# Kernel tuning notes

Hardware: AMD Instinct MI355X
Metric: run time of the kernel (lower is better)

## Reference

```python
import jax, jax.numpy as jnp
import numpy as np

NEG_SLOPE = 0.2


def _attn_layer(x, src, dst, W, a, n_nodes):
    # x: (N, Cin), W: (Cout, Cin) torch Linear convention, a: (2*Cout,)
    h = x @ W.T                                  # (N, Cout)
    H = h.shape[-1]
    # cat([x_i, x_j]) @ a  ==  h[dst] @ a[:H] + h[src] @ a[H:]
    s_i = h @ a[:H]                              # (N,)
    s_j = h @ a[H:]                              # (N,)
    score = s_i[dst] + s_j[src]                  # (E,)
    alpha = jax.nn.leaky_relu(score, NEG_SLOPE)
    # segment softmax over destination nodes
    amax = jax.ops.segment_max(alpha, dst, num_segments=n_nodes)
    amax = jnp.where(jnp.isfinite(amax), amax, 0.0)
    ex = jnp.exp(alpha - amax[dst])
    denom = jax.ops.segment_sum(ex, dst, num_segments=n_nodes)
    alpha = ex / denom[dst]                      # (E,)
    msg = h[src] * alpha[:, None]                # (E, Cout)
    sums = jax.ops.segment_sum(msg, dst, num_segments=n_nodes)
    cnt = jax.ops.segment_sum(jnp.ones_like(alpha), dst, num_segments=n_nodes)
    return sums / jnp.maximum(cnt, 1.0)[:, None]  # mean aggregation


def setup_inputs() -> dict:
    key = jax.random.key(0)
    ks = jax.random.split(key, 8)
    B, N, C, H, E = 16, 2048, 256, 256, 262144
    NT = B * N
    temporal_features = jax.random.normal(ks[0], (B, N, C), dtype=jnp.float32)
    edge_index = jax.random.randint(ks[1], (2, E), 0, NT, dtype=jnp.int64)
    sc = 1.0 / np.sqrt(C)
    W1 = jax.random.normal(ks[2], (H, C), dtype=jnp.float32) * sc
    a1 = jax.random.normal(ks[3], (2 * H,), dtype=jnp.float32) * sc
    W2 = jax.random.normal(ks[4], (H, H), dtype=jnp.float32) * sc
    a2 = jax.random.normal(ks[5], (2 * H,), dtype=jnp.float32) * sc
    W3 = jax.random.normal(ks[6], (H, H), dtype=jnp.float32) * sc
    a3 = jax.random.normal(ks[7], (2 * H,), dtype=jnp.float32) * sc
    return {"temporal_features": temporal_features, "edge_index": edge_index,
            "W1": W1, "a1": a1, "W2": W2, "a2": a2, "W3": W3, "a3": a3}


def reference(temporal_features, edge_index, W1, a1, W2, a2, W3, a3):
    B, N, C = temporal_features.shape
    n_nodes = B * N
    src, dst = edge_index[0], edge_index[1]  # x_j = x[src], x_i = x[dst]
    x = temporal_features.reshape(n_nodes, C)
    for W, a in ((W1, a1), (W2, a2), (W3, a3)):
        x = _attn_layer(x, src, dst, W, a, n_nodes)
        x = jax.nn.elu(x)
    return x.reshape(B, N, -1)
```

## Files before the change

kernel.cpp:

```cpp
#include <hip/hip_runtime.h>
#include <math.h>
#include <stdint.h>


typedef float f32x4 __attribute__((ext_vector_type(4)));
typedef _Float16 f16x8 __attribute__((ext_vector_type(8)));
typedef _Float16 f16x4 __attribute__((ext_vector_type(4)));


__global__ __launch_bounds__(256) void convert_f16(const float* __restrict__ src,
                                                   _Float16* __restrict__ dstp)
{
    const int i = (blockIdx.x * 256 + threadIdx.x) * 8;
    float4 a = *(const float4*)&src[i];
    float4 b = *(const float4*)&src[i + 4];
    f16x8 o = {(_Float16)a.x, (_Float16)a.y, (_Float16)a.z, (_Float16)a.w,
               (_Float16)b.x, (_Float16)b.y, (_Float16)b.z, (_Float16)b.w};
    *(f16x8*)&dstp[i] = o;
}


#define SWZ(row, byte) ((byte) ^ (((row) & 7) << 4))

__global__ __launch_bounds__(512) void gemm_f16(const _Float16* __restrict__ X,
                                                const _Float16* __restrict__ Wh,
                                                const float* __restrict__ avec,
                                                _Float16* __restrict__ Hout,
                                                float* __restrict__ si,
                                                float* __restrict__ sj)
{
    __shared__ __align__(16) unsigned char smem[49152];
    char* Xs = (char*)smem;
    char* Wl = (char*)smem + 16384;
    float (*Es)[260] = (float (*)[260])smem;

    const int tid  = threadIdx.x;
    const int lane = tid & 63;
    const int w    = tid >> 6;
    const int wr   = w >> 2;
    const int wc   = w & 3;
    const int ln   = lane & 15;
    const int kq   = lane >> 4;
    const int m0   = blockIdx.x * 128;

    const int xr = tid >> 2;
    const int xc = tid & 3;
    const int wrow = tid >> 1;
    const int wcb  = (tid & 1) * 64;

    const _Float16* Xg = X  + (size_t)(m0 + xr) * 256 + xc * 16;
    const _Float16* Wg = Wh + (size_t)wrow * 256 + wcb / 2;
    char* XsW = Xs + SWZ(xr, xr * 128 + xc * 32);
    char* XsW2 = Xs + SWZ(xr, xr * 128 + xc * 32 + 16);
    char* WlW0 = Wl + SWZ(wrow, wrow * 128 + wcb + 0);
    char* WlW1 = Wl + SWZ(wrow, wrow * 128 + wcb + 16);
    char* WlW2 = Wl + SWZ(wrow, wrow * 128 + wcb + 32);
    char* WlW3 = Wl + SWZ(wrow, wrow * 128 + wcb + 48);

    f32x4 acc[4][4] = {};

    for (int k0 = 0; k0 < 256; k0 += 64) {
        f16x8 x0 = *(const f16x8*)&Xg[k0];
        f16x8 x1 = *(const f16x8*)&Xg[k0 + 8];
        f16x8 w0 = *(const f16x8*)&Wg[k0];
        f16x8 w1 = *(const f16x8*)&Wg[k0 + 8];
        f16x8 w2 = *(const f16x8*)&Wg[k0 + 16];
        f16x8 w3 = *(const f16x8*)&Wg[k0 + 24];
        *(f16x8*)XsW  = x0;  *(f16x8*)XsW2 = x1;
        *(f16x8*)WlW0 = w0;  *(f16x8*)WlW1 = w1;
        *(f16x8*)WlW2 = w2;  *(f16x8*)WlW3 = w3;
        __syncthreads();

#pragma unroll
        for (int kk = 0; kk < 2; ++kk) {
            f16x8 af[4], bf[4];
#pragma unroll
            for (int i = 0; i < 4; ++i) {
                const int row = wr * 64 + i * 16 + ln;
                af[i] = *(const f16x8*)(Xs + SWZ(row, row * 128 + kk * 64 + kq * 16));
            }
#pragma unroll
            for (int j = 0; j < 4; ++j) {
                const int row = wc * 64 + j * 16 + ln;
                bf[j] = *(const f16x8*)(Wl + SWZ(row, row * 128 + kk * 64 + kq * 16));
            }
#pragma unroll
            for (int i = 0; i < 4; ++i)
#pragma unroll
                for (int j = 0; j < 4; ++j)
                    acc[i][j] = __builtin_amdgcn_mfma_f32_16x16x32_f16(af[i], bf[j], acc[i][j], 0, 0, 0);
        }
        __syncthreads();
    }

    const int er = tid >> 5;
    const int ec = tid & 31;
    for (int g = 0; g < 8; ++g) {
        if (wr == (g >> 2)) {
            const int i = g & 3;
#pragma unroll
            for (int j = 0; j < 4; ++j) {
                const int col = wc * 64 + j * 16 + ln;
#pragma unroll
                for (int q = 0; q < 4; ++q)
                    Es[kq * 4 + q][col] = acc[i][j][q];
            }
        }
        __syncthreads();
        const int grow = m0 + g * 16 + er;
        const int c0 = ec * 8;
        f32x4 v0 = *(const f32x4*)&Es[er][c0];
        f32x4 v1 = *(const f32x4*)&Es[er][c0 + 4];
        f16x8 ho = {(_Float16)v0[0], (_Float16)v0[1], (_Float16)v0[2], (_Float16)v0[3],
                    (_Float16)v1[0], (_Float16)v1[1], (_Float16)v1[2], (_Float16)v1[3]};
        *(f16x8*)&Hout[(size_t)grow * 256 + c0] = ho;

        f32x4 al0 = *(const f32x4*)&avec[c0];
        f32x4 al1 = *(const f32x4*)&avec[c0 + 4];
        f32x4 ah0 = *(const f32x4*)&avec[256 + c0];
        f32x4 ah1 = *(const f32x4*)&avec[256 + c0 + 4];
        float d0 = v0[0]*al0[0] + v0[1]*al0[1] + v0[2]*al0[2] + v0[3]*al0[3]
                 + v1[0]*al1[0] + v1[1]*al1[1] + v1[2]*al1[2] + v1[3]*al1[3];
        float d1 = v0[0]*ah0[0] + v0[1]*ah0[1] + v0[2]*ah0[2] + v0[3]*ah0[3]
                 + v1[0]*ah1[0] + v1[1]*ah1[1] + v1[2]*ah1[2] + v1[3]*ah1[3];
#pragma unroll
        for (int d = 16; d; d >>= 1) {
            d0 += __shfl_xor(d0, d);
            d1 += __shfl_xor(d1, d);
        }
        if (ec == 0) { si[grow] = d0; sj[grow] = d1; }
        __syncthreads();
    }
}


__global__ void zero_int(int* p, int n)
{
    int i = blockIdx.x * blockDim.x + threadIdx.x;
    if (i < n) p[i] = 0;
}

__global__ void hist_kernel(const int* __restrict__ dst, int* __restrict__ cnt, int E)
{
    int e = blockIdx.x * blockDim.x + threadIdx.x;
    if (e < E) atomicAdd(&cnt[dst[e]], 1);
}

__global__ __launch_bounds__(1024) void scan_part(const int* __restrict__ cnt,
                                                  int* __restrict__ off,
                                                  int* __restrict__ bsum)
{
    __shared__ int buf[1024];
    const int tid = threadIdx.x;
    const int g = blockIdx.x * 1024 + tid;
    int v = cnt[g];
    buf[tid] = v;
    __syncthreads();
#pragma unroll
    for (int d = 1; d < 1024; d <<= 1) {
        int t = (tid >= d) ? buf[tid - d] : 0;
        __syncthreads();
        buf[tid] += t;
        __syncthreads();
    }
    off[g] = buf[tid] - v;
    if (tid == 1023) bsum[blockIdx.x] = buf[1023];
}

__global__ void scan_bsum(int* bsum, int nb)
{
    __shared__ int b[64];
    const int tid = threadIdx.x;
    b[tid] = (tid < nb) ? bsum[tid] : 0;
    __syncthreads();
    if (tid == 0) {
        int a = 0;
        for (int i = 0; i < nb; ++i) { int t = b[i]; b[i] = a; a += t; }
    }
    __syncthreads();
    if (tid < nb) bsum[tid] = b[tid];
}

__global__ __launch_bounds__(1024) void scan_add(const int* __restrict__ bsum,
                                                 int* __restrict__ off,
                                                 int* __restrict__ cursor,
                                                 int NT, int E)
{
    const int tid = threadIdx.x;
    const int g = blockIdx.x * 1024 + tid;
    int v = off[g] + bsum[blockIdx.x];
    off[g] = v;
    cursor[g] = v;
    if (g == 0) off[NT] = E;
}

__global__ void scatter_kernel(const int* __restrict__ src,
                               const int* __restrict__ dst,
                               int* __restrict__ cursor,
                               int* __restrict__ ssrc, int E)
{
    int e = blockIdx.x * blockDim.x + threadIdx.x;
    if (e < E) {
        int p = atomicAdd(&cursor[dst[e]], 1);
        ssrc[p] = src[e];
    }
}


__device__ __forceinline__ float bcast_f(float x, int l)
{
    return __uint_as_float(__builtin_amdgcn_readlane(__float_as_uint(x), l));
}

template <int F16OUT>
__global__ __launch_bounds__(256) void aggregate(const _Float16* __restrict__ Hh,
                                                 const float* __restrict__ si,
                                                 const float* __restrict__ sj,
                                                 const int* __restrict__ off,
                                                 const int* __restrict__ ssrc,
                                                 void* __restrict__ outv,
                                                 int n_nodes)
{
    const int v = (blockIdx.x * 256 + threadIdx.x) >> 6;
    const int lane = threadIdx.x & 63;
    if (v >= n_nodes) return;

    const int e0 = off[v], e1 = off[v + 1];
    const int deg = e1 - e0;
    f32x4 acc = {0.f, 0.f, 0.f, 0.f};

    if (deg > 0 && deg <= 64) {
        const float siv = si[v];
        const int idx = e0 + lane;
        const bool on = idx < e1;
        int s = 0;
        float scv = -1e30f;
        if (on) {
            s = ssrc[idx];
            float t = siv + sj[s];
            scv = (t >= 0.f) ? t : 0.2f * t;
        }
        float m = scv;
#pragma unroll
        for (int d = 32; d; d >>= 1) m = fmaxf(m, __shfl_xor(m, d));
        float wv = on ? __expf(scv - m) : 0.f;
        float den = wv;
#pragma unroll
        for (int d = 32; d; d >>= 1) den += __shfl_xor(den, d);

        const int c4 = lane * 4;
        for (int eo = 0; eo < deg; eo += 4) {
            const int l1 = (eo + 1 < 63) ? eo + 1 : 63;
            const int l2 = (eo + 2 < 63) ? eo + 2 : 63;
            const int l3 = (eo + 3 < 63) ? eo + 3 : 63;
            const int s0 = __builtin_amdgcn_readlane(s, eo);
            const int s1 = __builtin_amdgcn_readlane(s, l1);
            const int s2 = __builtin_amdgcn_readlane(s, l2);
            const int s3 = __builtin_amdgcn_readlane(s, l3);
            const float w0 = bcast_f(wv, eo);
            const float w1 = bcast_f(wv, l1);
            const float w2 = bcast_f(wv, l2);
            const float w3 = bcast_f(wv, l3);
            const f16x4 v0 = *(const f16x4*)&Hh[(size_t)s0 * 256 + c4];
            const f16x4 v1 = *(const f16x4*)&Hh[(size_t)s1 * 256 + c4];
            const f16x4 v2 = *(const f16x4*)&Hh[(size_t)s2 * 256 + c4];
            const f16x4 v3 = *(const f16x4*)&Hh[(size_t)s3 * 256 + c4];
#pragma unroll
            for (int q = 0; q < 4; ++q)
                acc[q] += w0 * (float)v0[q] + w1 * (float)v1[q]
                        + w2 * (float)v2[q] + w3 * (float)v3[q];
        }
        const float inv = 1.f / (den * (float)deg);
#pragma unroll
        for (int q = 0; q < 4; ++q) acc[q] *= inv;
    } else if (deg > 64) {
        const float siv = si[v];
        float m = -1e30f;
        for (int b = e0 + lane; b < e1; b += 64) {
            float t = siv + sj[ssrc[b]];
            t = (t >= 0.f) ? t : 0.2f * t;
            m = fmaxf(m, t);
        }
#pragma unroll
        for (int d = 32; d; d >>= 1) m = fmaxf(m, __shfl_xor(m, d));
        float den = 0.f;
        for (int b = e0 + lane; b < e1; b += 64) {
            float t = siv + sj[ssrc[b]];
            t = (t >= 0.f) ? t : 0.2f * t;
            den += __expf(t - m);
        }
#pragma unroll
        for (int d = 32; d; d >>= 1) den += __shfl_xor(den, d);
        for (int e = e0; e < e1; ++e) {
            const int s = ssrc[e];
            float t = siv + sj[s];
            t = (t >= 0.f) ? t : 0.2f * t;
            const float wgt = __expf(t - m);
            const f16x4 hv = *(const f16x4*)&Hh[(size_t)s * 256 + lane * 4];
#pragma unroll
            for (int q = 0; q < 4; ++q) acc[q] += wgt * (float)hv[q];
        }
        const float inv = 1.f / (den * (float)deg);
#pragma unroll
        for (int q = 0; q < 4; ++q) acc[q] *= inv;
    }

    float4 o;
    o.x = (acc[0] > 0.f) ? acc[0] : (__expf(acc[0]) - 1.f);
    o.y = (acc[1] > 0.f) ? acc[1] : (__expf(acc[1]) - 1.f);
    o.z = (acc[2] > 0.f) ? acc[2] : (__expf(acc[2]) - 1.f);
    o.w = (acc[3] > 0.f) ? acc[3] : (__expf(acc[3]) - 1.f);
    if (F16OUT) {
        f16x4 oh = {(_Float16)o.x, (_Float16)o.y, (_Float16)o.z, (_Float16)o.w};
        *(f16x4*)&((_Float16*)outv)[(size_t)v * 256 + lane * 4] = oh;
    } else {
        *(float4*)&((float*)outv)[(size_t)v * 256 + lane * 4] = o;
    }
}


extern "C" void kernel_launch(void* const* d_in, const int* in_sizes, int n_in,
                              void* d_out, int out_size, void* d_ws, size_t ws_size,
                              hipStream_t stream)
{
    const float* x0 = (const float*)d_in[0];
    const int*   ei = (const int*)d_in[1];
    const float* Ws[3] = {(const float*)d_in[2], (const float*)d_in[4], (const float*)d_in[6]};
    const float* as[3] = {(const float*)d_in[3], (const float*)d_in[5], (const float*)d_in[7]};
    float* out = (float*)d_out;

    const int NT = in_sizes[0] / 256;
    const int E  = in_sizes[1] / 2;
    const int* srcI = ei;
    const int* dstI = ei + E;

    _Float16* Hh = (_Float16*)d_ws;
    _Float16* Xh = Hh + (size_t)NT * 256;
    float* si    = (float*)(Xh + (size_t)NT * 256);
    float* sj    = si + NT;
    int* cnt     = (int*)(sj + NT);
    int* off     = cnt + NT;
    int* cursor  = off + NT + 1;
    int* ssrc    = cursor + NT;
    int* bsum    = ssrc + E;
    _Float16* Wh = (_Float16*)(((uintptr_t)(bsum + 64) + 255) & ~(uintptr_t)255);

    for (int l = 0; l < 3; ++l)
        convert_f16<<<32, 256, 0, stream>>>(Ws[l], Wh + (size_t)l * 65536);
    convert_f16<<<NT * 256 / 2048, 256, 0, stream>>>(x0, Xh);

    zero_int<<<(NT + 255) / 256, 256, 0, stream>>>(cnt, NT);
    hist_kernel<<<(E + 255) / 256, 256, 0, stream>>>(dstI, cnt, E);
    scan_part<<<NT / 1024, 1024, 0, stream>>>(cnt, off, bsum);
    scan_bsum<<<1, 64, 0, stream>>>(bsum, NT / 1024);
    scan_add<<<NT / 1024, 1024, 0, stream>>>(bsum, off, cursor, NT, E);
    scatter_kernel<<<(E + 255) / 256, 256, 0, stream>>>(srcI, dstI, cursor, ssrc, E);

    for (int l = 0; l < 3; ++l) {
        gemm_f16<<<NT / 128, 512, 0, stream>>>(Xh, Wh + (size_t)l * 65536, as[l], Hh, si, sj);
        if (l < 2)
            aggregate<1><<<NT / 4, 256, 0, stream>>>(Hh, si, sj, off, ssrc, (void*)Xh, NT);
        else
            aggregate<0><<<NT / 4, 256, 0, stream>>>(Hh, si, sj, off, ssrc, (void*)out, NT);
    }
}
```

Baseline: 249.0 us.

## Double-buffer GEMM shared-memory tiles and merge conversion kernels into one launch

The GEMM k-loop now prefetches the next 64-wide K slice from global memory into registers while MFMAs run on the current LDS buffer, then writes it into a second LDS buffer. This leaves one barrier per iteration instead of two and overlaps global loads with compute. Shared memory per block doubles to 96 KB, which may reduce occupancy. The four fp32-to-fp16 conversion launches are merged into one kernel to cut launch overhead.

```diff
diff --git a/kernel.cpp b/kernel.cpp
--- a/kernel.cpp
+++ b/kernel.cpp
@@ -8,15 +8,29 @@
 typedef _Float16 f16x4 __attribute__((ext_vector_type(4)));
 
 
-__global__ __launch_bounds__(256) void convert_f16(const float* __restrict__ src,
-                                                   _Float16* __restrict__ dstp)
+__global__ __launch_bounds__(256) void convert_all(const float* __restrict__ x0,
+                                                   _Float16* __restrict__ Xh, int nx,
+                                                   const float* __restrict__ W0,
+                                                   const float* __restrict__ W1,
+                                                   const float* __restrict__ W2,
+                                                   _Float16* __restrict__ Wh)
 {
     const int i = (blockIdx.x * 256 + threadIdx.x) * 8;
-    float4 a = *(const float4*)&src[i];
-    float4 b = *(const float4*)&src[i + 4];
+    const float* src;
+    _Float16* dstp;
+    int off;
+    if (i < nx) { src = x0; dstp = Xh; off = i; }
+    else {
+        const int j = i - nx;
+        src = (j < 65536) ? W0 : ((j < 131072) ? W1 : W2);
+        off = j & 65535;
+        dstp = Wh + (j - off);
+    }
+    float4 a = *(const float4*)&src[off];
+    float4 b = *(const float4*)&src[off + 4];
     f16x8 o = {(_Float16)a.x, (_Float16)a.y, (_Float16)a.z, (_Float16)a.w,
                (_Float16)b.x, (_Float16)b.y, (_Float16)b.z, (_Float16)b.w};
-    *(f16x8*)&dstp[i] = o;
+    *(f16x8*)&dstp[off] = o;
 }
 
 
@@ -29,9 +43,7 @@
                                                 float* __restrict__ si,
                                                 float* __restrict__ sj)
 {
-    __shared__ __align__(16) unsigned char smem[49152];
-    char* Xs = (char*)smem;
-    char* Wl = (char*)smem + 16384;
+    __shared__ __align__(16) unsigned char smem[98304];
     float (*Es)[260] = (float (*)[260])smem;
 
     const int tid  = threadIdx.x;
@@ -50,45 +62,62 @@
 
     const _Float16* Xg = X  + (size_t)(m0 + xr) * 256 + xc * 16;
     const _Float16* Wg = Wh + (size_t)wrow * 256 + wcb / 2;
-    char* XsW = Xs + SWZ(xr, xr * 128 + xc * 32);
-    char* XsW2 = Xs + SWZ(xr, xr * 128 + xc * 32 + 16);
-    char* WlW0 = Wl + SWZ(wrow, wrow * 128 + wcb + 0);
-    char* WlW1 = Wl + SWZ(wrow, wrow * 128 + wcb + 16);
-    char* WlW2 = Wl + SWZ(wrow, wrow * 128 + wcb + 32);
-    char* WlW3 = Wl + SWZ(wrow, wrow * 128 + wcb + 48);
+    const int xs0 = SWZ(xr, xr * 128 + xc * 32);
+    const int xs1 = SWZ(xr, xr * 128 + xc * 32 + 16);
+    const int wl0 = 16384 + SWZ(wrow, wrow * 128 + wcb + 0);
+    const int wl1 = 16384 + SWZ(wrow, wrow * 128 + wcb + 16);
+    const int wl2 = 16384 + SWZ(wrow, wrow * 128 + wcb + 32);
+    const int wl3 = 16384 + SWZ(wrow, wrow * 128 + wcb + 48);
 
     f32x4 acc[4][4] = {};
 
-    for (int k0 = 0; k0 < 256; k0 += 64) {
-        f16x8 x0 = *(const f16x8*)&Xg[k0];
-        f16x8 x1 = *(const f16x8*)&Xg[k0 + 8];
-        f16x8 w0 = *(const f16x8*)&Wg[k0];
-        f16x8 w1 = *(const f16x8*)&Wg[k0 + 8];
-        f16x8 w2 = *(const f16x8*)&Wg[k0 + 16];
-        f16x8 w3 = *(const f16x8*)&Wg[k0 + 24];
-        *(f16x8*)XsW  = x0;  *(f16x8*)XsW2 = x1;
-        *(f16x8*)WlW0 = w0;  *(f16x8*)WlW1 = w1;
-        *(f16x8*)WlW2 = w2;  *(f16x8*)WlW3 = w3;
-        __syncthreads();
-
+    f16x8 x0 = *(const f16x8*)&Xg[0];
+    f16x8 x1 = *(const f16x8*)&Xg[8];
+    f16x8 w0 = *(const f16x8*)&Wg[0];
+    f16x8 w1 = *(const f16x8*)&Wg[8];
+    f16x8 w2 = *(const f16x8*)&Wg[16];
+    f16x8 w3 = *(const f16x8*)&Wg[24];
+    *(f16x8*)(smem + xs0) = x0;  *(f16x8*)(smem + xs1) = x1;
+    *(f16x8*)(smem + wl0) = w0;  *(f16x8*)(smem + wl1) = w1;
+    *(f16x8*)(smem + wl2) = w2;  *(f16x8*)(smem + wl3) = w3;
+    __syncthreads();
+
+#pragma unroll
+    for (int t = 0; t < 4; ++t) {
+        const int cb = (t & 1) * 49152;
+        const int nb = ((t & 1) ^ 1) * 49152;
+        if (t < 3) {
+            const int k0 = (t + 1) * 64;
+            x0 = *(const f16x8*)&Xg[k0];
+            x1 = *(const f16x8*)&Xg[k0 + 8];
+            w0 = *(const f16x8*)&Wg[k0];
+            w1 = *(const f16x8*)&Wg[k0 + 8];
+            w2 = *(const f16x8*)&Wg[k0 + 16];
+            w3 = *(const f16x8*)&Wg[k0 + 24];
+        }
 #pragma unroll
         for (int kk = 0; kk < 2; ++kk) {
             f16x8 af[4], bf[4];
 #pragma unroll
             for (int i = 0; i < 4; ++i) {
                 const int row = wr * 64 + i * 16 + ln;
-                af[i] = *(const f16x8*)(Xs + SWZ(row, row * 128 + kk * 64 + kq * 16));
+                af[i] = *(const f16x8*)(smem + cb + SWZ(row, row * 128 + kk * 64 + kq * 16));
             }
 #pragma unroll
             for (int j = 0; j < 4; ++j) {
                 const int row = wc * 64 + j * 16 + ln;
-                bf[j] = *(const f16x8*)(Wl + SWZ(row, row * 128 + kk * 64 + kq * 16));
+                bf[j] = *(const f16x8*)(smem + cb + 16384 + SWZ(row, row * 128 + kk * 64 + kq * 16));
             }
 #pragma unroll
             for (int i = 0; i < 4; ++i)
 #pragma unroll
                 for (int j = 0; j < 4; ++j)
                     acc[i][j] = __builtin_amdgcn_mfma_f32_16x16x32_f16(af[i], bf[j], acc[i][j], 0, 0, 0);
+        }
+        if (t < 3) {
+            *(f16x8*)(smem + nb + xs0) = x0;  *(f16x8*)(smem + nb + xs1) = x1;
+            *(f16x8*)(smem + nb + wl0) = w0;  *(f16x8*)(smem + nb + wl1) = w1;
+            *(f16x8*)(smem + nb + wl2) = w2;  *(f16x8*)(smem + nb + wl3) = w3;
         }
         __syncthreads();
     }
@@ -345,9 +374,9 @@
     int* bsum    = ssrc + E;
     _Float16* Wh = (_Float16*)(((uintptr_t)(bsum + 64) + 255) & ~(uintptr_t)255);
 
-    for (int l = 0; l < 3; ++l)
-        convert_f16<<<32, 256, 0, stream>>>(Ws[l], Wh + (size_t)l * 65536);
-    convert_f16<<<NT * 256 / 2048, 256, 0, stream>>>(x0, Xh);
+    const int nx = NT * 256;
+    convert_all<<<(nx + 3 * 65536) / 2048, 256, 0, stream>>>(x0, Xh, nx,
+                                                             Ws[0], Ws[1], Ws[2], Wh);
 
     zero_int<<<(NT + 255) / 256, 256, 0, stream>>>(cnt, NT);
     hist_kernel<<<(E + 255) / 256, 256, 0, stream>>>(dstI, cnt, E);
```

Measured after the change: 241.5 us. 3.0% less time.
